# Optimization experiments

Hardware: AMD Instinct MI355X
Metric: run time of the kernel (lower is better)

Reference implementation:

```python
import jax, jax.numpy as jnp
import numpy as np

L = 4       # num_fourier_layers
W = 256     # width
NF = 256    # num_freq (no_low_freq)
B = 2       # batch size
N = 16384   # num_nodes per graph
E = 524288  # total edges (avg degree 16)
D_IN = 3    # darcy input features


def lin(x, w, b):
    # torch nn.Linear convention: w is (out, in)
    return x @ w.T + b


def layernorm(x, s, b):
    m = x.mean(-1, keepdims=True)
    v = x.var(-1, keepdims=True)
    return (x - m) / jnp.sqrt(v + 1e-5) * s + b


def setup_inputs() -> dict:
    key = jax.random.key(0)
    ks = jax.random.split(key, 16)
    s = lambda i, shape, sc=0.05: sc * jax.random.normal(ks[i], shape, jnp.float32)
    inp = {
        "x": jax.random.normal(ks[0], (B * N, D_IN), jnp.float32),
        "U": jax.random.normal(ks[1], (B, N, NF), jnp.float32) / np.float32(np.sqrt(N)),
        "edge_index": jax.random.randint(ks[2], (2, E), 0, B * N),
        "edge_weight": jax.random.uniform(ks[3], (E,), jnp.float32),
        "lif_embed": jax.random.normal(ks[4], (B * N, 16), jnp.float32),
        "p_w": s(5, (W, D_IN)), "p_b": jnp.zeros((W,), jnp.float32),
        # scale = 1/(in*out) * rand, per GraphFourierLayer
        "four_w": (1.0 / (W * W)) * jax.random.uniform(ks[6], (L, W, W, NF), jnp.float32),
        "w_w": s(7, (L, W, W)), "w_b": jnp.zeros((L, W), jnp.float32),
        "ln_s": jnp.ones((L, W), jnp.float32), "ln_b": jnp.zeros((L, W), jnp.float32),
        "lin_w": s(8, (L, W, W)), "lin_b": jnp.zeros((L, W), jnp.float32),
        "ew_w": s(9, (L, 16, 1)), "ew_b": jnp.zeros((L, 16), jnp.float32),
        "g1_w": s(10, (L, 3, 48)), "g1_b": jnp.zeros((L, 3), jnp.float32),
        "g2_w": s(11, (L, 1, 3)), "g2_b": jnp.zeros((L, 1), jnp.float32),
        "proj_w": s(12, (W, 2 * W)), "proj_b": jnp.zeros((W,), jnp.float32),
        "q1_w": s(13, (128, W)), "q1_b": jnp.zeros((128,), jnp.float32),
        "q2_w": s(14, (1, 128)), "q2_b": jnp.zeros((1,), jnp.float32),
    }
    return inp


def reference(x, U, edge_index, edge_weight, lif_embed,
              p_w, p_b, four_w, w_w, w_b, ln_s, ln_b,
              lin_w, lin_b, ew_w, ew_b, g1_w, g1_b, g2_w, g2_b,
              proj_w, proj_b, q1_w, q1_b, q2_w, q2_b):
    src = edge_index[0]  # edge_index_j (source)
    dst = edge_index[1]  # edge_index_i (target, aggr='add')
    h = lin(x, p_w, p_b)  # [B*N, W]

    for l in range(L):
        # --- GraphFourierLayer: batched spectral transform ---
        h3 = h.reshape(B, N, W)
        x_ft = jnp.einsum('bnf,bnw->bfw', U, h3)          # U^T x  -> [B, NF, W]
        out_ft = jnp.einsum('bfi,iof->bfo', x_ft, four_w[l])
        x1 = jnp.einsum('bnf,bfw->bnw', U, out_ft).reshape(B * N, W)
        xf = jax.nn.gelu(x1 + lin(h, w_w[l], w_b[l]), approximate=False)
        xf = layernorm(xf, ln_s[l], ln_b[l])

        # --- FrigateConv: gather -> edge MLP gate -> scatter-add -> L2 normalize ---
        xs = lin(h, lin_w[l], lin_b[l])
        ew = lin(edge_weight[:, None], ew_w[l], ew_b[l])  # [E, 16]
        gin = jnp.concatenate([ew, lif_embed[dst], lif_embed[src]], axis=1)  # [E, 48]
        g = jax.nn.sigmoid(lin(jax.nn.relu(lin(gin, g1_w[l], g1_b[l])), g2_w[l], g2_b[l]))
        msg = xs[src] * g                                  # [E, W]
        agg = jax.ops.segment_sum(msg, dst, num_segments=B * N)
        nrm = jnp.maximum(jnp.linalg.norm(agg, axis=-1, keepdims=True), 1e-12)
        xs = agg / nrm

        h = lin(jnp.concatenate([xf, xs], axis=1), proj_w, proj_b)

    out = lin(jax.nn.relu(lin(h, q1_w, q1_b)), q2_w, q2_b)  # q: MLP(W,1,128)
    return out
```

## Files before the change

kernel.cpp:

```cpp
#include <hip/hip_runtime.h>
#include <hip/hip_bf16.h>

#define B_ 2
#define N_ 16384
#define BN 32768
#define W_ 256
#define NF_ 256
#define E_ 524288
#define L_ 4
#define KS_ 32

typedef __attribute__((ext_vector_type(8))) short bf16x8;
typedef __attribute__((ext_vector_type(4))) float f32x4;

__device__ __forceinline__ unsigned short f2b(float x) {
    __hip_bfloat16 h = __float2bfloat16(x);
    return *reinterpret_cast<unsigned short*>(&h);
}
__device__ __forceinline__ float b2f(unsigned short u) {
    union { unsigned int i; float f; } c; c.i = ((unsigned int)u) << 16; return c.f;
}
__device__ __forceinline__ float geluf(float x) {
    return 0.5f * x * (1.0f + erff(x * 0.70710678118654752440f));
}

template<bool DUAL, int OUTM, bool BIAS, bool QHEAD = false, bool TROUT = false>
__global__ __launch_bounds__(256) void k_mfma_nt(
    const unsigned short* __restrict__ A1, int lda1, long A1o, long A1i,
    const unsigned short* __restrict__ B1, int ldb1, long B1o, long B1i, int K1,
    const unsigned short* __restrict__ A2, int lda2, long A2o,
    const unsigned short* __restrict__ B2, int ldb2, long B2o, int K2,
    void* __restrict__ Cv, int ldc, long Co, long Ci,
    unsigned short* __restrict__ CT,
    const float* __restrict__ bias,
    const float* __restrict__ qw, const float* __restrict__ q2b,
    float* __restrict__ qout, int zdiv)
{
    __shared__ unsigned short lds[16384];
    const int t = threadIdx.x;
    const int wid = t >> 6, lane = t & 63;
    const int wr = wid >> 1, wc = wid & 1;
    const int m0 = blockIdx.y * 128, n0 = blockIdx.x * 128;
    const int z = blockIdx.z;
    const int zo = z / zdiv, zi = z - zo * zdiv;
    A1 += zo * A1o + zi * A1i;
    B1 += zo * B1o + zi * B1i;
    if (DUAL) { A2 += zo * A2o; B2 += zo * B2o; }

    const int srow  = t >> 3;
    const int sgran = (t & 7) ^ (srow & 7);
    const int rlo   = lane & 15;
    const int hi    = lane >> 4;

    f32x4 acc[4][4] = {};

    const int nph = DUAL ? 2 : 1;
    for (int ph = 0; ph < nph; ++ph) {
        const unsigned short* A  = (DUAL && ph) ? A2 : A1;
        const unsigned short* Bp = (DUAL && ph) ? B2 : B1;
        const int lda = (DUAL && ph) ? lda2 : lda1;
        const int ldb = (DUAL && ph) ? ldb2 : ldb1;
        const int K   = (DUAL && ph) ? K2 : K1;
        for (int k0 = 0; k0 < K; k0 += 64) {
            __syncthreads();
            #pragma unroll
            for (int j = 0; j < 4; ++j) {
                const unsigned short* ga = A + (long)(m0 + j*32 + srow) * lda + k0 + sgran*8;
                __builtin_amdgcn_global_load_lds(
                    (const __attribute__((address_space(1))) void*)ga,
                    (__attribute__((address_space(3))) void*)&lds[(j*4 + wid) * 512],
                    16, 0, 0);
            }
            #pragma unroll
            for (int j = 0; j < 4; ++j) {
                const unsigned short* gb = Bp + (long)(n0 + j*32 + srow) * ldb + k0 + sgran*8;
                __builtin_amdgcn_global_load_lds(
                    (const __attribute__((address_space(1))) void*)gb,
                    (__attribute__((address_space(3))) void*)&lds[8192 + (j*4 + wid) * 512],
                    16, 0, 0);
            }
            __syncthreads();
            #pragma unroll
            for (int kk = 0; kk < 2; ++kk) {
                const int g8 = (((kk*4 + hi) ^ (lane & 7)) << 3);
                bf16x8 a[4], b[4];
                #pragma unroll
                for (int fm = 0; fm < 4; ++fm)
                    a[fm] = *(const bf16x8*)&lds[(wr*64 + fm*16 + rlo)*64 + g8];
                #pragma unroll
                for (int fn = 0; fn < 4; ++fn)
                    b[fn] = *(const bf16x8*)&lds[8192 + (wc*64 + fn*16 + rlo)*64 + g8];
                #pragma unroll
                for (int fm = 0; fm < 4; ++fm)
                    #pragma unroll
                    for (int fn = 0; fn < 4; ++fn)
                        acc[fm][fn] = __builtin_amdgcn_mfma_f32_16x16x32_bf16(
                            a[fm], b[fn], acc[fm][fn], 0, 0, 0);
            }
        }
    }

    const int mb = m0 + wr*64, nb = n0 + wc*64;
    if (QHEAD) {
        __syncthreads();
        float* rs = (float*)lds;
        if (t < 128) rs[t] = 0.f;
        __syncthreads();
        #pragma unroll
        for (int fm = 0; fm < 4; ++fm)
            #pragma unroll
            for (int r = 0; r < 4; ++r) {
                const int m_l = wr*64 + fm*16 + hi*4 + r;
                float part = 0.f;
                #pragma unroll
                for (int fn = 0; fn < 4; ++fn) {
                    const int n = nb + fn*16 + rlo;
                    part += fmaxf(acc[fm][fn][r] + bias[n], 0.f) * qw[n];
                }
                #pragma unroll
                for (int o = 8; o; o >>= 1) part += __shfl_xor(part, o);
                if (rlo == 0) atomicAdd(&rs[m_l], part);
            }
        __syncthreads();
        if (t < 128) qout[m0 + t] = rs[t] + q2b[0];
    } else if (OUTM == 1) {
        unsigned short* C = (unsigned short*)Cv + zo * Co + zi * Ci;
        #pragma unroll
        for (int fn = 0; fn < 4; ++fn) {
            const int n = nb + fn*16 + rlo;
            const float bv = BIAS ? bias[n] : 0.f;
            #pragma unroll
            for (int fm = 0; fm < 4; ++fm)
                #pragma unroll
                for (int r = 0; r < 4; ++r) {
                    const int m = mb + fm*16 + hi*4 + r;
                    C[(long)m*ldc + n] = f2b(acc[fm][fn][r] + bv);
                }
        }
        if (TROUT) {
            __syncthreads();
            unsigned short* wlds = &lds[wid * 4096];
            #pragma unroll
            for (int fm = 0; fm < 4; ++fm)
                #pragma unroll
                for (int r = 0; r < 4; ++r) {
                    const int m_l = fm*16 + hi*4 + r;
                    const int sw = (m_l & 7) << 3;
                    #pragma unroll
                    for (int fn = 0; fn < 4; ++fn) {
                        const int n_l = fn*16 + rlo;
                        const float bv = BIAS ? bias[nb + n_l] : 0.f;
                        wlds[m_l*64 + (n_l ^ sw)] = f2b(acc[fm][fn][r] + bv);
                    }
                }
            const int bb = mb >> 14, loc = mb & 16383;
            const int mq = lane & 15, nq = lane >> 4;
            #pragma unroll
            for (int p = 0; p < 16; ++p) {
                const int n_l = p*4 + nq;
                unsigned short v[4];
                #pragma unroll
                for (int j = 0; j < 4; ++j) {
                    const int m_l = mq*4 + j;
                    v[j] = wlds[m_l*64 + (n_l ^ ((m_l & 7) << 3))];
                }
                *(ushort4*)&CT[((long)bb*ldc + nb + n_l)*N_ + loc + mq*4] = *(ushort4*)v;
            }
        }
    } else {
        float* C = (float*)Cv + zo * Co + zi * Ci;
        #pragma unroll
        for (int fn = 0; fn < 4; ++fn) {
            const int n = nb + fn*16 + rlo;
            const float bv = BIAS ? bias[n] : 0.f;
            #pragma unroll
            for (int fm = 0; fm < 4; ++fm)
                #pragma unroll
                for (int r = 0; r < 4; ++r) {
                    const int m = mb + fm*16 + hi*4 + r;
                    C[(long)m*ldc + n] = acc[fm][fn][r] + bv;
                }
        }
    }
}

__global__ __launch_bounds__(256) void k_spec_xs(
    const unsigned short* __restrict__ hT, const unsigned short* __restrict__ UT,
    float* __restrict__ xft_part,
    const unsigned short* __restrict__ h, const unsigned short* __restrict__ linw,
    const float* __restrict__ lin_b, unsigned short* __restrict__ xs)
{
    __shared__ unsigned short lds[16384];
    const int t = threadIdx.x;
    const int wid = t >> 6, lane = t & 63;
    const int wr = wid >> 1, wc = wid & 1;
    const int srow  = t >> 3;
    const int sgran = (t & 7) ^ (srow & 7);
    const int rlo   = lane & 15;
    const int hi    = lane >> 4;
    const int blk = blockIdx.x;

    if (blk < 256) {
        const int bx = blk & 1, by = (blk >> 1) & 1, z = blk >> 2;
        const int zo = z / KS_, zi = z - zo * KS_;
        const unsigned short* A  = hT + (long)zo * W_ * N_ + (long)zi * (N_ / KS_);
        const unsigned short* Bp = UT + (long)zo * NF_ * N_ + (long)zi * (N_ / KS_);
        const int m0 = by * 128, n0 = bx * 128;
        f32x4 acc[4][4] = {};
        for (int k0 = 0; k0 < N_/KS_; k0 += 64) {
            __syncthreads();
            #pragma unroll
            for (int j = 0; j < 4; ++j) {
                const unsigned short* ga = A + (long)(m0 + j*32 + srow) * N_ + k0 + sgran*8;
                __builtin_amdgcn_global_load_lds(
                    (const __attribute__((address_space(1))) void*)ga,
                    (__attribute__((address_space(3))) void*)&lds[(j*4 + wid) * 512], 16, 0, 0);
                const unsigned short* gb = Bp + (long)(n0 + j*32 + srow) * N_ + k0 + sgran*8;
                __builtin_amdgcn_global_load_lds(
                    (const __attribute__((address_space(1))) void*)gb,
                    (__attribute__((address_space(3))) void*)&lds[8192 + (j*4 + wid) * 512], 16, 0, 0);
            }
            __syncthreads();
            #pragma unroll
            for (int kk = 0; kk < 2; ++kk) {
                const int g8 = (((kk*4 + hi) ^ (lane & 7)) << 3);
                bf16x8 a[4], b[4];
                #pragma unroll
                for (int fm = 0; fm < 4; ++fm)
                    a[fm] = *(const bf16x8*)&lds[(wr*64 + fm*16 + rlo)*64 + g8];
                #pragma unroll
                for (int fn = 0; fn < 4; ++fn)
                    b[fn] = *(const bf16x8*)&lds[8192 + (wc*64 + fn*16 + rlo)*64 + g8];
                #pragma unroll
                for (int fm = 0; fm < 4; ++fm)
                    #pragma unroll
                    for (int fn = 0; fn < 4; ++fn)
                        acc[fm][fn] = __builtin_amdgcn_mfma_f32_16x16x32_bf16(
                            a[fm], b[fn], acc[fm][fn], 0, 0, 0);
            }
        }
        float* C = xft_part + (long)zo * KS_ * 65536 + (long)zi * 65536;
        const int mb = m0 + wr*64, nb = n0 + wc*64;
        #pragma unroll
        for (int fn = 0; fn < 4; ++fn) {
            const int n = nb + fn*16 + rlo;
            #pragma unroll
            for (int fm = 0; fm < 4; ++fm)
                #pragma unroll
                for (int r = 0; r < 4; ++r) {
                    const int m = mb + fm*16 + hi*4 + r;
                    C[(long)m*NF_ + n] = acc[fm][fn][r];
                }
        }
    } else {
        const int idx = blk - 256;
        const int bx = idx & 1, by = idx >> 1;
        const int m0 = by * 128, n0 = bx * 128;
        f32x4 acc[4][4] = {};
        for (int k0 = 0; k0 < W_; k0 += 64) {
            __syncthreads();
            #pragma unroll
            for (int j = 0; j < 4; ++j) {
                const unsigned short* ga = h + (long)(m0 + j*32 + srow) * W_ + k0 + sgran*8;
                __builtin_amdgcn_global_load_lds(
                    (const __attribute__((address_space(1))) void*)ga,
                    (__attribute__((address_space(3))) void*)&lds[(j*4 + wid) * 512], 16, 0, 0);
                const unsigned short* gb = linw + (long)(n0 + j*32 + srow) * W_ + k0 + sgran*8;
                __builtin_amdgcn_global_load_lds(
                    (const __attribute__((address_space(1))) void*)gb,
                    (__attribute__((address_space(3))) void*)&lds[8192 + (j*4 + wid) * 512], 16, 0, 0);
            }
            __syncthreads();
            #pragma unroll
            for (int kk = 0; kk < 2; ++kk) {
                const int g8 = (((kk*4 + hi) ^ (lane & 7)) << 3);
                bf16x8 a[4], b[4];
                #pragma unroll
                for (int fm = 0; fm < 4; ++fm)
                    a[fm] = *(const bf16x8*)&lds[(wr*64 + fm*16 + rlo)*64 + g8];
                #pragma unroll
                for (int fn = 0; fn < 4; ++fn)
                    b[fn] = *(const bf16x8*)&lds[8192 + (wc*64 + fn*16 + rlo)*64 + g8];
                #pragma unroll
                for (int fm = 0; fm < 4; ++fm)
                    #pragma unroll
                    for (int fn = 0; fn < 4; ++fn)
                        acc[fm][fn] = __builtin_amdgcn_mfma_f32_16x16x32_bf16(
                            a[fm], b[fn], acc[fm][fn], 0, 0, 0);
            }
        }
        const int mb = m0 + wr*64, nb = n0 + wc*64;
        #pragma unroll
        for (int fn = 0; fn < 4; ++fn) {
            const int n = nb + fn*16 + rlo;
            const float lb = lin_b[n];
            #pragma unroll
            for (int fm = 0; fm < 4; ++fm)
                #pragma unroll
                for (int r = 0; r < 4; ++r) {
                    const int m = mb + fm*16 + hi*4 + r;
                    xs[(long)m*W_ + n] = f2b(acc[fm][fn][r] + lb);
                }
        }
    }
}

__global__ __launch_bounds__(256) void k_four_gate(
    const float* __restrict__ fw, const float* __restrict__ xftT,
    unsigned short* __restrict__ oftT,
    const int* __restrict__ offsets, const int* __restrict__ srcp,
    const float* __restrict__ ewt_p, const float* __restrict__ lif,
    const float* __restrict__ eww, const float* __restrict__ ewb,
    const float* __restrict__ g1w, const float* __restrict__ g1b,
    const float* __restrict__ g2w, const float* __restrict__ g2b,
    const unsigned short* __restrict__ xs, unsigned short* __restrict__ xsn)
{
    const int lane = threadIdx.x & 63;
    if (blockIdx.x < 256) {
        const int o = blockIdx.x, f = threadIdx.x;
        const float* fwp = fw + (long)o * NF_ + f;
        float a0 = 0.f, a1 = 0.f;
        #pragma unroll 8
        for (int i = 0; i < W_; ++i) {
            float w = fwp[(long)i * W_ * NF_];
            a0 = fmaf(xftT[i*NF_ + f], w, a0);
            a1 = fmaf(xftT[65536 + i*NF_ + f], w, a1);
        }
        oftT[o*NF_ + f] = f2b(a0);
        oftT[65536 + o*NF_ + f] = f2b(a1);
    } else {
        const int node = (blockIdx.x - 256) * 4 + (threadIdx.x >> 6);
        const int beg = offsets[node], end = offsets[node + 1];
        float lifd[16];
        #pragma unroll
        for (int j = 0; j < 16; ++j) lifd[j] = lif[node*16 + j];
        float a0=0.f, a1=0.f, a2=0.f, a3=0.f;
        for (int c0 = beg; c0 < end; c0 += 64) {
            const int p = c0 + lane;
            float gate = 0.f; int src = 0;
            if (p < end) {
                src = srcp[p];
                const float wv = ewt_p[p];
                float t0 = g1b[0], t1 = g1b[1], t2 = g1b[2];
                #pragma unroll
                for (int j = 0; j < 16; ++j) {
                    const float e0 = fmaf(wv, eww[j], ewb[j]);
                    const float l1 = lifd[j];
                    const float l2 = lif[src*16 + j];
                    t0 = fmaf(g1w[j], e0, t0);
                    t0 = fmaf(g1w[16 + j], l1, t0);
                    t0 = fmaf(g1w[32 + j], l2, t0);
                    t1 = fmaf(g1w[48 + j], e0, t1);
                    t1 = fmaf(g1w[64 + j], l1, t1);
                    t1 = fmaf(g1w[80 + j], l2, t1);
                    t2 = fmaf(g1w[96 + j], e0, t2);
                    t2 = fmaf(g1w[112 + j], l1, t2);
                    t2 = fmaf(g1w[128 + j], l2, t2);
                }
                float z = g2b[0];
                z = fmaf(g2w[0], fmaxf(t0, 0.f), z);
                z = fmaf(g2w[1], fmaxf(t1, 0.f), z);
                z = fmaf(g2w[2], fmaxf(t2, 0.f), z);
                gate = 1.f / (1.f + __expf(-z));
            }
            const int m = min(64, end - c0);
            for (int j = 0; j < m; ++j) {
                const float gv = __shfl(gate, j);
                const int   s  = __shfl(src, j);
                ushort4 v = *(const ushort4*)&xs[(long)s * W_ + lane * 4];
                a0 = fmaf(b2f(v.x), gv, a0);
                a1 = fmaf(b2f(v.y), gv, a1);
                a2 = fmaf(b2f(v.z), gv, a2);
                a3 = fmaf(b2f(v.w), gv, a3);
            }
        }
        float s = a0*a0 + a1*a1 + a2*a2 + a3*a3;
        #pragma unroll
        for (int o = 32; o; o >>= 1) s += __shfl_xor(s, o);
        float inv = 1.f / fmaxf(sqrtf(s), 1e-12f);
        ushort4 r = {f2b(a0*inv), f2b(a1*inv), f2b(a2*inv), f2b(a3*inv)};
        *(ushort4*)(xsn + (long)node * W_ + lane * 4) = r;
    }
}

__global__ __launch_bounds__(256) void k_prologue(
    const float* __restrict__ w_w, const float* __restrict__ lin_w,
    const float* __restrict__ proj_w, const float* __restrict__ q1_w,
    unsigned short* __restrict__ wwb, unsigned short* __restrict__ linwb,
    unsigned short* __restrict__ projwb, unsigned short* __restrict__ q1wb,
    const float* __restrict__ U, unsigned short* __restrict__ UT, unsigned short* __restrict__ UL,
    const float* __restrict__ x, const float* __restrict__ pw, const float* __restrict__ pb,
    unsigned short* __restrict__ h, unsigned short* __restrict__ hT)
{
    __shared__ unsigned short tile[64][72];
    const int blk = blockIdx.x;
    const int t = threadIdx.x;
    if (blk < 672) {
        const float* s; unsigned short* d; long base;
        if (blk < 256)      { s = w_w;    d = wwb;    base = (long)blk * 1024; }
        else if (blk < 512) { s = lin_w;  d = linwb;  base = (long)(blk-256) * 1024; }
        else if (blk < 640) { s = proj_w; d = projwb; base = (long)(blk-512) * 1024; }
        else                { s = q1_w;   d = q1wb;   base = (long)(blk-640) * 1024; }
        long i = base + (long)t * 4;
        float4 v = *(const float4*)&s[i];
        ushort4 u = {f2b(v.x), f2b(v.y), f2b(v.z), f2b(v.w)};
        *(ushort4*)&d[i] = u;
    } else if (blk < 2720) {
        const int lb = blk - 672;
        const int b = lb >> 10;
        const int rem = lb & 1023;
        const int cy = rem >> 2, cx = rem & 3;
        const float* src = U + (long)b * N_ * NF_;
        unsigned short* dT = UT + (long)b * N_ * NF_;
        unsigned short* dL = UL + (long)b * N_ * NF_;
        const int r0 = cy * 64, c0 = cx * 64;
        const int lr = t >> 4, lc4 = (t & 15) * 4;
        #pragma unroll
        for (int p = 0; p < 4; ++p) {
            int r = p*16 + lr;
            float4 v = *(const float4*)&src[(long)(r0+r)*NF_ + c0 + lc4];
            ushort4 u = {f2b(v.x), f2b(v.y), f2b(v.z), f2b(v.w)};
            *(ushort4*)&dL[(long)(r0+r)*NF_ + c0 + lc4] = u;
            tile[r][lc4+0]=u.x; tile[r][lc4+1]=u.y; tile[r][lc4+2]=u.z; tile[r][lc4+3]=u.w;
        }
        __syncthreads();
        #pragma unroll
        for (int p = 0; p < 4; ++p) {
            int c = p*16 + lr;
            ushort4 u = {tile[lc4+0][c], tile[lc4+1][c], tile[lc4+2][c], tile[lc4+3][c]};
            *(ushort4*)&dT[(long)(c0+c)*N_ + r0 + lc4] = u;
        }
    } else {
        const int lb = blk - 2720;
        const int b = lb >> 10;
        const int rem = lb & 1023;
        const int ry = rem >> 2, rx = rem & 3;
        const int r0 = ry * 64, c0 = rx * 64;
        const int lr = t >> 4, lc4 = (t & 15) * 4;
        float pwv[12], pbv4[4];
        #pragma unroll
        for (int j = 0; j < 4; ++j) {
            const int w = c0 + lc4 + j;
            pwv[j*3+0] = pw[w*3+0]; pwv[j*3+1] = pw[w*3+1]; pwv[j*3+2] = pw[w*3+2];
            pbv4[j] = pb[w];
        }
        #pragma unroll
        for (int p = 0; p < 4; ++p) {
            const int r = p*16 + lr;
            const float* xr = x + (long)(b*N_ + r0 + r) * 3;
            const float x0 = xr[0], x1 = xr[1], x2 = xr[2];
            ushort4 u;
            u.x = f2b(fmaf(x0,pwv[0],fmaf(x1,pwv[1],fmaf(x2,pwv[2],pbv4[0]))));
            u.y = f2b(fmaf(x0,pwv[3],fmaf(x1,pwv[4],fmaf(x2,pwv[5],pbv4[1]))));
            u.z = f2b(fmaf(x0,pwv[6],fmaf(x1,pwv[7],fmaf(x2,pwv[8],pbv4[2]))));
            u.w = f2b(fmaf(x0,pwv[9],fmaf(x1,pwv[10],fmaf(x2,pwv[11],pbv4[3]))));
            *(ushort4*)&h[(long)(b*N_ + r0 + r)*W_ + c0 + lc4] = u;
            tile[r][lc4+0]=u.x; tile[r][lc4+1]=u.y; tile[r][lc4+2]=u.z; tile[r][lc4+3]=u.w;
        }
        __syncthreads();
        #pragma unroll
        for (int p = 0; p < 4; ++p) {
            const int c = p*16 + lr;
            ushort4 u = {tile[lc4+0][c], tile[lc4+1][c], tile[lc4+2][c], tile[lc4+3][c]};
            *(ushort4*)&hT[((long)b*W_ + c0 + c)*N_ + r0 + lc4] = u;
        }
    }
}

__global__ __launch_bounds__(256) void k_reduce_ks(
    const float* __restrict__ part, float* __restrict__ outp)
{
    int idx = blockIdx.x * 256 + threadIdx.x;
    int b = idx >> 16, rem = idx & 65535;
    const float* p = part + (long)b * KS_ * 65536 + rem;
    float s = 0.f;
    #pragma unroll 16
    for (int k = 0; k < KS_; ++k) s += p[(long)k * 65536];
    outp[idx] = s;
}

__global__ __launch_bounds__(256) void k_gelu_ln(
    const unsigned short* __restrict__ xf, unsigned short* __restrict__ out,
    const float* __restrict__ wb, const float* __restrict__ lns, const float* __restrict__ lnb)
{
    const int node = blockIdx.x * 4 + (threadIdx.x >> 6);
    const int lane = threadIdx.x & 63;
    ushort4 v4 = *(const ushort4*)(xf + (long)node*W_ + lane*4);
    float4 bb = *(const float4*)(wb + lane*4);
    float e0 = geluf(b2f(v4.x)+bb.x), e1 = geluf(b2f(v4.y)+bb.y);
    float e2 = geluf(b2f(v4.z)+bb.z), e3 = geluf(b2f(v4.w)+bb.w);
    float s  = e0+e1+e2+e3;
    float s2 = e0*e0+e1*e1+e2*e2+e3*e3;
    #pragma unroll
    for (int o = 32; o; o >>= 1) { s += __shfl_xor(s, o); s2 += __shfl_xor(s2, o); }
    float mean = s * (1.0f/W_);
    float var  = s2 * (1.0f/W_) - mean*mean;
    float inv = rsqrtf(var + 1e-5f);
    float4 sc = *(const float4*)(lns + lane*4);
    float4 bi = *(const float4*)(lnb + lane*4);
    ushort4 o4;
    o4.x = f2b((e0-mean)*inv*sc.x + bi.x);
    o4.y = f2b((e1-mean)*inv*sc.y + bi.y);
    o4.z = f2b((e2-mean)*inv*sc.z + bi.z);
    o4.w = f2b((e3-mean)*inv*sc.w + bi.w);
    *(ushort4*)(out + (long)node*W_ + lane*4) = o4;
}

__global__ __launch_bounds__(256) void k_hist(const int* __restrict__ ei, int* __restrict__ count) {
    int e = blockIdx.x * 256 + threadIdx.x;
    atomicAdd(&count[ei[E_ + e]], 1);
}
__global__ __launch_bounds__(1024) void k_scan(const int* __restrict__ count, int* __restrict__ offsets) {
    __shared__ int sums[1024];
    const int t = threadIdx.x;
    const int base = t * 32;
    int s = 0;
    #pragma unroll
    for (int i = 0; i < 32; ++i) s += count[base + i];
    sums[t] = s;
    __syncthreads();
    for (int off = 1; off < 1024; off <<= 1) {
        int v = (t >= off) ? sums[t - off] : 0;
        __syncthreads();
        sums[t] += v;
        __syncthreads();
    }
    int run = (t == 0) ? 0 : sums[t - 1];
    #pragma unroll
    for (int i = 0; i < 32; ++i) { offsets[base + i] = run; run += count[base + i]; }
    if (t == 1023) offsets[BN] = run;
}
__global__ __launch_bounds__(256) void k_place(
    const int* __restrict__ ei, const float* __restrict__ ewt,
    const int* __restrict__ offsets, int* __restrict__ cursor,
    int* __restrict__ srcp, float* __restrict__ ewt_p)
{
    int e = blockIdx.x * 256 + threadIdx.x;
    int dst = ei[E_ + e];
    int pos = offsets[dst] + atomicAdd(&cursor[dst], 1);
    srcp[pos] = ei[e];
    ewt_p[pos] = ewt[e];
}

extern "C" void kernel_launch(void* const* d_in, const int* in_sizes, int n_in,
                              void* d_out, int out_size, void* d_ws, size_t ws_size,
                              hipStream_t stream)
{
    const float* x      = (const float*)d_in[0];
    const float* U      = (const float*)d_in[1];
    const int*   ei     = (const int*)  d_in[2];
    const float* ewt    = (const float*)d_in[3];
    const float* lif    = (const float*)d_in[4];
    const float* p_w    = (const float*)d_in[5];
    const float* p_b    = (const float*)d_in[6];
    const float* four_w = (const float*)d_in[7];
    const float* w_w    = (const float*)d_in[8];
    const float* w_b    = (const float*)d_in[9];
    const float* ln_s   = (const float*)d_in[10];
    const float* ln_b   = (const float*)d_in[11];
    const float* lin_w  = (const float*)d_in[12];
    const float* lin_b  = (const float*)d_in[13];
    const float* ew_w   = (const float*)d_in[14];
    const float* ew_b   = (const float*)d_in[15];
    const float* g1_w   = (const float*)d_in[16];
    const float* g1_b   = (const float*)d_in[17];
    const float* g2_w   = (const float*)d_in[18];
    const float* g2_b   = (const float*)d_in[19];
    const float* proj_w = (const float*)d_in[20];
    const float* proj_b = (const float*)d_in[21];
    const float* q1_w   = (const float*)d_in[22];
    const float* q1_b   = (const float*)d_in[23];
    const float* q2_w   = (const float*)d_in[24];
    const float* q2_b   = (const float*)d_in[25];

    char* wsb = (char*)d_ws;
    size_t off = 0;
    auto alloc = [&](size_t bytes) -> void* {
        void* p = wsb + off; off += (bytes + 255) & ~(size_t)255; return p;
    };
    float* xft_part  = (float*)alloc((size_t)B_ * KS_ * 65536 * 4);
    float* xftT      = (float*)alloc((size_t)B_ * 65536 * 4);
    unsigned short* h_bf   = (unsigned short*)alloc((size_t)BN * W_ * 2);
    unsigned short* hT_bf  = (unsigned short*)alloc((size_t)BN * W_ * 2);
    unsigned short* U_bf   = (unsigned short*)alloc((size_t)BN * NF_ * 2);
    unsigned short* UT_bf  = (unsigned short*)alloc((size_t)BN * NF_ * 2);
    unsigned short* xfg    = (unsigned short*)alloc((size_t)BN * W_ * 2);
    unsigned short* xf_bf  = (unsigned short*)alloc((size_t)BN * W_ * 2);
    unsigned short* xs_bf  = (unsigned short*)alloc((size_t)BN * W_ * 2);
    unsigned short* xsn_bf = (unsigned short*)alloc((size_t)BN * W_ * 2);
    unsigned short* oftT_bf= (unsigned short*)alloc((size_t)B_ * 65536 * 2);
    unsigned short* wwb    = (unsigned short*)alloc((size_t)L_ * W_ * W_ * 2);
    unsigned short* linwb  = (unsigned short*)alloc((size_t)L_ * W_ * W_ * 2);
    unsigned short* projwb = (unsigned short*)alloc((size_t)W_ * 2 * W_ * 2);
    unsigned short* q1wb   = (unsigned short*)alloc((size_t)128 * W_ * 2);
    int*   srcp    = (int*)alloc((size_t)E_ * 4);
    float* ewt_p   = (float*)alloc((size_t)E_ * 4);
    int*   count   = (int*)alloc((size_t)BN * 4);
    int*   cursor  = (int*)alloc((size_t)BN * 4);
    int*   offsets = (int*)alloc((size_t)(BN + 1) * 4);

    hipMemsetAsync(count, 0, (size_t)2 * BN * 4, stream);
    k_hist<<<E_/256, 256, 0, stream>>>(ei, count);
    k_scan<<<1, 1024, 0, stream>>>(count, offsets);
    k_place<<<E_/256, 256, 0, stream>>>(ei, ewt, offsets, cursor, srcp, ewt_p);

    k_prologue<<<4768, 256, 0, stream>>>(
        w_w, lin_w, proj_w, q1_w, wwb, linwb, projwb, q1wb,
        U, UT_bf, U_bf,
        x, p_w, p_b, h_bf, hT_bf);

    for (int l = 0; l < L_; ++l) {
        k_spec_xs<<<768, 256, 0, stream>>>(
            hT_bf, UT_bf, xft_part,
            h_bf, linwb + (long)l*W_*W_, lin_b + l*W_, xs_bf);
        k_reduce_ks<<<(B_*65536)/256, 256, 0, stream>>>(xft_part, xftT);
        k_four_gate<<<256 + BN/4, 256, 0, stream>>>(
            four_w + (long)l*W_*W_*NF_, xftT, oftT_bf,
            offsets, srcp, ewt_p, lif,
            ew_w + l*16, ew_b + l*16, g1_w + l*144, g1_b + l*3,
            g2_w + l*3, g2_b + l, xs_bf, xsn_bf);
        k_mfma_nt<true,1,false><<<dim3(2, N_/128, B_), 256, 0, stream>>>(
            U_bf, NF_, (long)N_*NF_, 0,
            oftT_bf, NF_, (long)65536, 0, NF_,
            h_bf, W_, (long)N_*W_,
            wwb + (long)l*W_*W_, W_, 0, W_,
            xfg, W_, (long)N_*W_, 0,
            nullptr, nullptr, nullptr, nullptr, nullptr, 1);
        k_gelu_ln<<<BN/4, 256, 0, stream>>>(xfg, xf_bf, w_b + l*W_, ln_s + l*W_, ln_b + l*W_);
        if (l < 3) {
            k_mfma_nt<true,1,true,false,true><<<dim3(2, BN/128, 1), 256, 0, stream>>>(
                xf_bf, W_, 0, 0,
                projwb, 2*W_, 0, 0, W_,
                xsn_bf, W_, 0,
                projwb + W_, 2*W_, 0, W_,
                h_bf, W_, 0, 0,
                hT_bf, proj_b, nullptr, nullptr, nullptr, 1);
        } else {
            k_mfma_nt<true,1,true><<<dim3(2, BN/128, 1), 256, 0, stream>>>(
                xf_bf, W_, 0, 0,
                projwb, 2*W_, 0, 0, W_,
                xsn_bf, W_, 0,
                projwb + W_, 2*W_, 0, W_,
                h_bf, W_, 0, 0,
                nullptr, proj_b, nullptr, nullptr, nullptr, 1);
        }
    }
    k_mfma_nt<false,0,true,true><<<dim3(1, BN/128, 1), 256, 0, stream>>>(
        h_bf, W_, 0, 0,
        q1wb, W_, 0, 0, W_,
        nullptr, 0, 0, nullptr, 0, 0, 0,
        nullptr, 128, 0, 0,
        nullptr, q1_b, q2_w, q2_b, (float*)d_out, 1);
}
```

Measured before the change: 698.1 us.

## Split gather-gate work across fourier-mix and xf GEMM kernels for overlap

```diff
diff --git a/kernel.cpp b/kernel.cpp
--- a/kernel.cpp
+++ b/kernel.cpp
@@ -22,6 +22,67 @@
 }
 __device__ __forceinline__ float geluf(float x) {
     return 0.5f * x * (1.0f + erff(x * 0.70710678118654752440f));
+}
+
+__device__ __forceinline__ void gate_agg_node(
+    int node, int lane,
+    const int* __restrict__ offsets, const int* __restrict__ srcp,
+    const float* __restrict__ ewt_p, const float* __restrict__ lif,
+    const float* __restrict__ eww, const float* __restrict__ ewb,
+    const float* __restrict__ g1w, const float* __restrict__ g1b,
+    const float* __restrict__ g2w, const float* __restrict__ g2b,
+    const unsigned short* __restrict__ xs, unsigned short* __restrict__ xsn)
+{
+    const int beg = offsets[node], end = offsets[node + 1];
+    float lifd[16];
+    #pragma unroll
+    for (int j = 0; j < 16; ++j) lifd[j] = lif[node*16 + j];
+    float a0=0.f, a1=0.f, a2=0.f, a3=0.f;
+    for (int c0 = beg; c0 < end; c0 += 64) {
+        const int p = c0 + lane;
+        float gate = 0.f; int src = 0;
+        if (p < end) {
+            src = srcp[p];
+            const float wv = ewt_p[p];
+            float t0 = g1b[0], t1 = g1b[1], t2 = g1b[2];
+            #pragma unroll
+            for (int j = 0; j < 16; ++j) {
+                const float e0 = fmaf(wv, eww[j], ewb[j]);
+                const float l1 = lifd[j];
+                const float l2 = lif[src*16 + j];
+                t0 = fmaf(g1w[j], e0, t0);
+                t0 = fmaf(g1w[16 + j], l1, t0);
+                t0 = fmaf(g1w[32 + j], l2, t0);
+                t1 = fmaf(g1w[48 + j], e0, t1);
+                t1 = fmaf(g1w[64 + j], l1, t1);
+                t1 = fmaf(g1w[80 + j], l2, t1);
+                t2 = fmaf(g1w[96 + j], e0, t2);
+                t2 = fmaf(g1w[112 + j], l1, t2);
+                t2 = fmaf(g1w[128 + j], l2, t2);
+            }
+            float z = g2b[0];
+            z = fmaf(g2w[0], fmaxf(t0, 0.f), z);
+            z = fmaf(g2w[1], fmaxf(t1, 0.f), z);
+            z = fmaf(g2w[2], fmaxf(t2, 0.f), z);
+            gate = 1.f / (1.f + __expf(-z));
+        }
+        const int m = min(64, end - c0);
+        for (int j = 0; j < m; ++j) {
+            const float gv = __shfl(gate, j);
+            const int   s  = __shfl(src, j);
+            ushort4 v = *(const ushort4*)&xs[(long)s * W_ + lane * 4];
+            a0 = fmaf(b2f(v.x), gv, a0);
+            a1 = fmaf(b2f(v.y), gv, a1);
+            a2 = fmaf(b2f(v.z), gv, a2);
+            a3 = fmaf(b2f(v.w), gv, a3);
+        }
+    }
+    float s = a0*a0 + a1*a1 + a2*a2 + a3*a3;
+    #pragma unroll
+    for (int o = 32; o; o >>= 1) s += __shfl_xor(s, o);
+    float inv = 1.f / fmaxf(sqrtf(s), 1e-12f);
+    ushort4 r = {f2b(a0*inv), f2b(a1*inv), f2b(a2*inv), f2b(a3*inv)};
+    *(ushort4*)(xsn + (long)node * W_ + lane * 4) = r;
 }
 
 template<bool DUAL, int OUTM, bool BIAS, bool QHEAD = false, bool TROUT = false>
@@ -330,56 +391,93 @@
         oftT[65536 + o*NF_ + f] = f2b(a1);
     } else {
         const int node = (blockIdx.x - 256) * 4 + (threadIdx.x >> 6);
-        const int beg = offsets[node], end = offsets[node + 1];
-        float lifd[16];
-        #pragma unroll
-        for (int j = 0; j < 16; ++j) lifd[j] = lif[node*16 + j];
-        float a0=0.f, a1=0.f, a2=0.f, a3=0.f;
-        for (int c0 = beg; c0 < end; c0 += 64) {
-            const int p = c0 + lane;
-            float gate = 0.f; int src = 0;
-            if (p < end) {
-                src = srcp[p];
-                const float wv = ewt_p[p];
-                float t0 = g1b[0], t1 = g1b[1], t2 = g1b[2];
-                #pragma unroll
-                for (int j = 0; j < 16; ++j) {
-                    const float e0 = fmaf(wv, eww[j], ewb[j]);
-                    const float l1 = lifd[j];
-                    const float l2 = lif[src*16 + j];
-                    t0 = fmaf(g1w[j], e0, t0);
-                    t0 = fmaf(g1w[16 + j], l1, t0);
-                    t0 = fmaf(g1w[32 + j], l2, t0);
-                    t1 = fmaf(g1w[48 + j], e0, t1);
-                    t1 = fmaf(g1w[64 + j], l1, t1);
-                    t1 = fmaf(g1w[80 + j], l2, t1);
-                    t2 = fmaf(g1w[96 + j], e0, t2);
-                    t2 = fmaf(g1w[112 + j], l1, t2);
-                    t2 = fmaf(g1w[128 + j], l2, t2);
-                }
-                float z = g2b[0];
-                z = fmaf(g2w[0], fmaxf(t0, 0.f), z);
-                z = fmaf(g2w[1], fmaxf(t1, 0.f), z);
-                z = fmaf(g2w[2], fmaxf(t2, 0.f), z);
-                gate = 1.f / (1.f + __expf(-z));
-            }
-            const int m = min(64, end - c0);
-            for (int j = 0; j < m; ++j) {
-                const float gv = __shfl(gate, j);
-                const int   s  = __shfl(src, j);
-                ushort4 v = *(const ushort4*)&xs[(long)s * W_ + lane * 4];
-                a0 = fmaf(b2f(v.x), gv, a0);
-                a1 = fmaf(b2f(v.y), gv, a1);
-                a2 = fmaf(b2f(v.z), gv, a2);
-                a3 = fmaf(b2f(v.w), gv, a3);
-            }
-        }
-        float s = a0*a0 + a1*a1 + a2*a2 + a3*a3;
-        #pragma unroll
-        for (int o = 32; o; o >>= 1) s += __shfl_xor(s, o);
-        float inv = 1.f / fmaxf(sqrtf(s), 1e-12f);
-        ushort4 r = {f2b(a0*inv), f2b(a1*inv), f2b(a2*inv), f2b(a3*inv)};
-        *(ushort4*)(xsn + (long)node * W_ + lane * 4) = r;
+        gate_agg_node(node, lane, offsets, srcp, ewt_p, lif,
+                      eww, ewb, g1w, g1b, g2w, g2b, xs, xsn);
+    }
+}
+
+__global__ __launch_bounds__(256) void k_xf_gate(
+    const unsigned short* __restrict__ Ubf, const unsigned short* __restrict__ oftT,
+    const unsigned short* __restrict__ h, const unsigned short* __restrict__ ww,
+    unsigned short* __restrict__ xfg,
+    const int* __restrict__ offsets, const int* __restrict__ srcp,
+    const float* __restrict__ ewt_p, const float* __restrict__ lif,
+    const float* __restrict__ eww, const float* __restrict__ ewb,
+    const float* __restrict__ g1w, const float* __restrict__ g1b,
+    const float* __restrict__ g2w, const float* __restrict__ g2b,
+    const unsigned short* __restrict__ xs, unsigned short* __restrict__ xsn)
+{
+    __shared__ unsigned short lds[16384];
+    const int blk = blockIdx.x;
+    const int t = threadIdx.x;
+    const int lane = t & 63;
+    if (blk < 512) {
+        const int wid = t >> 6;
+        const int wr = wid >> 1, wc = wid & 1;
+        const int bx = blk & 1, by = (blk >> 1) & 127, b = blk >> 8;
+        const int m0 = by * 128, n0 = bx * 128;
+        const unsigned short* A1 = Ubf  + (long)b * N_ * NF_;
+        const unsigned short* B1 = oftT + (long)b * 65536;
+        const unsigned short* A2 = h    + (long)b * N_ * W_;
+        const int srow  = t >> 3;
+        const int sgran = (t & 7) ^ (srow & 7);
+        const int rlo   = lane & 15;
+        const int hi    = lane >> 4;
+        f32x4 acc[4][4] = {};
+        #pragma unroll
+        for (int ph = 0; ph < 2; ++ph) {
+            const unsigned short* A  = ph ? A2 : A1;
+            const unsigned short* Bp = ph ? ww : B1;
+            for (int k0 = 0; k0 < 256; k0 += 64) {
+                __syncthreads();
+                #pragma unroll
+                for (int j = 0; j < 4; ++j) {
+                    const unsigned short* ga = A + (long)(m0 + j*32 + srow) * 256 + k0 + sgran*8;
+                    __builtin_amdgcn_global_load_lds(
+                        (const __attribute__((address_space(1))) void*)ga,
+                        (__attribute__((address_space(3))) void*)&lds[(j*4 + wid) * 512], 16, 0, 0);
+                    const unsigned short* gb = Bp + (long)(n0 + j*32 + srow) * 256 + k0 + sgran*8;
+                    __builtin_amdgcn_global_load_lds(
+                        (const __attribute__((address_space(1))) void*)gb,
+                        (__attribute__((address_space(3))) void*)&lds[8192 + (j*4 + wid) * 512], 16, 0, 0);
+                }
+                __syncthreads();
+                #pragma unroll
+                for (int kk = 0; kk < 2; ++kk) {
+                    const int g8 = (((kk*4 + hi) ^ (lane & 7)) << 3);
+                    bf16x8 a[4], b[4];
+                    #pragma unroll
+                    for (int fm = 0; fm < 4; ++fm)
+                        a[fm] = *(const bf16x8*)&lds[(wr*64 + fm*16 + rlo)*64 + g8];
+                    #pragma unroll
+                    for (int fn = 0; fn < 4; ++fn)
+                        b[fn] = *(const bf16x8*)&lds[8192 + (wc*64 + fn*16 + rlo)*64 + g8];
+                    #pragma unroll
+                    for (int fm = 0; fm < 4; ++fm)
+                        #pragma unroll
+                        for (int fn = 0; fn < 4; ++fn)
+                            acc[fm][fn] = __builtin_amdgcn_mfma_f32_16x16x32_bf16(
+                                a[fm], b[fn], acc[fm][fn], 0, 0, 0);
+                }
+            }
+        }
+        unsigned short* C = xfg + (long)b * N_ * W_;
+        const int mb = m0 + wr*64, nb = n0 + wc*64;
+        #pragma unroll
+        for (int fn = 0; fn < 4; ++fn) {
+            const int n = nb + fn*16 + rlo;
+            #pragma unroll
+            for (int fm = 0; fm < 4; ++fm)
+                #pragma unroll
+                for (int r = 0; r < 4; ++r) {
+                    const int m = mb + fm*16 + hi*4 + r;
+                    C[(long)m*W_ + n] = f2b(acc[fm][fn][r]);
+                }
+        }
+    } else {
+        const int node = BN/2 + (blk - 512) * 4 + (t >> 6);
+        gate_agg_node(node, lane, offsets, srcp, ewt_p, lif,
+                      eww, ewb, g1w, g1b, g2w, g2b, xs, xsn);
     }
 }
 
@@ -614,18 +712,16 @@
             hT_bf, UT_bf, xft_part,
             h_bf, linwb + (long)l*W_*W_, lin_b + l*W_, xs_bf);
         k_reduce_ks<<<(B_*65536)/256, 256, 0, stream>>>(xft_part, xftT);
-        k_four_gate<<<256 + BN/4, 256, 0, stream>>>(
+        k_four_gate<<<256 + BN/8, 256, 0, stream>>>(
             four_w + (long)l*W_*W_*NF_, xftT, oftT_bf,
             offsets, srcp, ewt_p, lif,
             ew_w + l*16, ew_b + l*16, g1_w + l*144, g1_b + l*3,
             g2_w + l*3, g2_b + l, xs_bf, xsn_bf);
-        k_mfma_nt<true,1,false><<<dim3(2, N_/128, B_), 256, 0, stream>>>(
-            U_bf, NF_, (long)N_*NF_, 0,
-            oftT_bf, NF_, (long)65536, 0, NF_,
-            h_bf, W_, (long)N_*W_,
-            wwb + (long)l*W_*W_, W_, 0, W_,
-            xfg, W_, (long)N_*W_, 0,
-            nullptr, nullptr, nullptr, nullptr, nullptr, 1);
+        k_xf_gate<<<512 + BN/8, 256, 0, stream>>>(
+            U_bf, oftT_bf, h_bf, wwb + (long)l*W_*W_, xfg,
+            offsets, srcp, ewt_p, lif,
+            ew_w + l*16, ew_b + l*16, g1_w + l*144, g1_b + l*3,
+            g2_w + l*3, g2_b + l, xs_bf, xsn_bf);
         k_gelu_ln<<<BN/4, 256, 0, stream>>>(xfg, xf_bf, w_b + l*W_, ln_s + l*W_, ln_b + l*W_);
         if (l < 3) {
             k_mfma_nt<true,1,true,false,true><<<dim3(2, BN/128, 1), 256, 0, stream>>>(
```

Result: slower. 872.0 us (+24.9%).

## Fuse spectral-inverse GEMM with GELU and LayerNorm into one full-row kernel

Applied to the files above, without the earlier changes.

```diff
diff --git a/kernel.cpp b/kernel.cpp
--- a/kernel.cpp
+++ b/kernel.cpp
@@ -182,6 +182,116 @@
                 }
         }
     }
+}
+
+__global__ __launch_bounds__(256) void k_xf_ln(
+    const unsigned short* __restrict__ Ubf, const unsigned short* __restrict__ oftT,
+    const unsigned short* __restrict__ h, const unsigned short* __restrict__ ww,
+    const float* __restrict__ wb, const float* __restrict__ lns, const float* __restrict__ lnb,
+    unsigned short* __restrict__ xf)
+{
+    __shared__ unsigned short lds[24576];
+    const int t = threadIdx.x;
+    const int wid = t >> 6, lane = t & 63;
+    const int m0 = blockIdx.x * 128;
+    const int b = blockIdx.y;
+    Ubf  += (long)b * N_ * NF_;
+    oftT += (long)b * 65536;
+    h    += (long)b * N_ * W_;
+
+    const int srow  = t >> 3;
+    const int sgran = (t & 7) ^ (srow & 7);
+    const int rlo   = lane & 15;
+    const int hi    = lane >> 4;
+
+    f32x4 acc[8][4] = {};
+
+    #pragma unroll
+    for (int ph = 0; ph < 2; ++ph) {
+        const unsigned short* A  = ph ? h  : Ubf;
+        const unsigned short* Bp = ph ? ww : oftT;
+        for (int k0 = 0; k0 < 256; k0 += 64) {
+            __syncthreads();
+            #pragma unroll
+            for (int j = 0; j < 4; ++j) {
+                const unsigned short* ga = A + (long)(m0 + j*32 + srow) * 256 + k0 + sgran*8;
+                __builtin_amdgcn_global_load_lds(
+                    (const __attribute__((address_space(1))) void*)ga,
+                    (__attribute__((address_space(3))) void*)&lds[(j*4 + wid) * 512], 16, 0, 0);
+            }
+            #pragma unroll
+            for (int j = 0; j < 8; ++j) {
+                const unsigned short* gb = Bp + (long)(j*32 + srow) * 256 + k0 + sgran*8;
+                __builtin_amdgcn_global_load_lds(
+                    (const __attribute__((address_space(1))) void*)gb,
+                    (__attribute__((address_space(3))) void*)&lds[8192 + (j*4 + wid) * 512], 16, 0, 0);
+            }
+            __syncthreads();
+            #pragma unroll
+            for (int kk = 0; kk < 2; ++kk) {
+                const int g8 = (((kk*4 + hi) ^ (lane & 7)) << 3);
+                bf16x8 bfr[4];
+                #pragma unroll
+                for (int fn = 0; fn < 4; ++fn)
+                    bfr[fn] = *(const bf16x8*)&lds[8192 + (wid*64 + fn*16 + rlo)*64 + g8];
+                #pragma unroll
+                for (int fm = 0; fm < 8; ++fm) {
+                    bf16x8 a = *(const bf16x8*)&lds[(fm*16 + rlo)*64 + g8];
+                    #pragma unroll
+                    for (int fn = 0; fn < 4; ++fn)
+                        acc[fm][fn] = __builtin_amdgcn_mfma_f32_16x16x32_bf16(
+                            a, bfr[fn], acc[fm][fn], 0, 0, 0);
+                }
+            }
+        }
+    }
+
+    float wbv[4], lsv[4], lbv[4];
+    #pragma unroll
+    for (int fn = 0; fn < 4; ++fn) {
+        const int c = wid*64 + fn*16 + rlo;
+        wbv[fn] = wb[c]; lsv[fn] = lns[c]; lbv[fn] = lnb[c];
+    }
+    __syncthreads();
+    float* sums  = (float*)lds;
+    float* sumsq = (float*)lds + 512;
+    #pragma unroll
+    for (int fm = 0; fm < 8; ++fm)
+        #pragma unroll
+        for (int r = 0; r < 4; ++r) {
+            float s = 0.f, s2 = 0.f;
+            #pragma unroll
+            for (int fn = 0; fn < 4; ++fn) {
+                const float g = geluf(acc[fm][fn][r] + wbv[fn]);
+                acc[fm][fn][r] = g;
+                s += g; s2 += g*g;
+            }
+            #pragma unroll
+            for (int o = 1; o < 16; o <<= 1) { s += __shfl_xor(s, o); s2 += __shfl_xor(s2, o); }
+            if (rlo == 0) {
+                const int row = fm*16 + hi*4 + r;
+                sums [row*4 + wid] = s;
+                sumsq[row*4 + wid] = s2;
+            }
+        }
+    __syncthreads();
+    #pragma unroll
+    for (int fm = 0; fm < 8; ++fm)
+        #pragma unroll
+        for (int r = 0; r < 4; ++r) {
+            const int row = fm*16 + hi*4 + r;
+            const float s  = sums [row*4+0] + sums [row*4+1] + sums [row*4+2] + sums [row*4+3];
+            const float s2 = sumsq[row*4+0] + sumsq[row*4+1] + sumsq[row*4+2] + sumsq[row*4+3];
+            const float mean = s * (1.0f/W_);
+            const float var  = s2 * (1.0f/W_) - mean*mean;
+            const float inv  = rsqrtf(var + 1e-5f);
+            const long mrow = (long)(b*N_ + m0 + row) * W_;
+            #pragma unroll
+            for (int fn = 0; fn < 4; ++fn) {
+                const int c = wid*64 + fn*16 + rlo;
+                xf[mrow + c] = f2b((acc[fm][fn][r] - mean)*inv*lsv[fn] + lbv[fn]);
+            }
+        }
 }
 
 __global__ __launch_bounds__(256) void k_spec_xs(
@@ -479,33 +589,6 @@
     outp[idx] = s;
 }
 
-__global__ __launch_bounds__(256) void k_gelu_ln(
-    const unsigned short* __restrict__ xf, unsigned short* __restrict__ out,
-    const float* __restrict__ wb, const float* __restrict__ lns, const float* __restrict__ lnb)
-{
-    const int node = blockIdx.x * 4 + (threadIdx.x >> 6);
-    const int lane = threadIdx.x & 63;
-    ushort4 v4 = *(const ushort4*)(xf + (long)node*W_ + lane*4);
-    float4 bb = *(const float4*)(wb + lane*4);
-    float e0 = geluf(b2f(v4.x)+bb.x), e1 = geluf(b2f(v4.y)+bb.y);
-    float e2 = geluf(b2f(v4.z)+bb.z), e3 = geluf(b2f(v4.w)+bb.w);
-    float s  = e0+e1+e2+e3;
-    float s2 = e0*e0+e1*e1+e2*e2+e3*e3;
-    #pragma unroll
-    for (int o = 32; o; o >>= 1) { s += __shfl_xor(s, o); s2 += __shfl_xor(s2, o); }
-    float mean = s * (1.0f/W_);
-    float var  = s2 * (1.0f/W_) - mean*mean;
-    float inv = rsqrtf(var + 1e-5f);
-    float4 sc = *(const float4*)(lns + lane*4);
-    float4 bi = *(const float4*)(lnb + lane*4);
-    ushort4 o4;
-    o4.x = f2b((e0-mean)*inv*sc.x + bi.x);
-    o4.y = f2b((e1-mean)*inv*sc.y + bi.y);
-    o4.z = f2b((e2-mean)*inv*sc.z + bi.z);
-    o4.w = f2b((e3-mean)*inv*sc.w + bi.w);
-    *(ushort4*)(out + (long)node*W_ + lane*4) = o4;
-}
-
 __global__ __launch_bounds__(256) void k_hist(const int* __restrict__ ei, int* __restrict__ count) {
     int e = blockIdx.x * 256 + threadIdx.x;
     atomicAdd(&count[ei[E_ + e]], 1);
@@ -584,7 +667,6 @@
     unsigned short* hT_bf  = (unsigned short*)alloc((size_t)BN * W_ * 2);
     unsigned short* U_bf   = (unsigned short*)alloc((size_t)BN * NF_ * 2);
     unsigned short* UT_bf  = (unsigned short*)alloc((size_t)BN * NF_ * 2);
-    unsigned short* xfg    = (unsigned short*)alloc((size_t)BN * W_ * 2);
     unsigned short* xf_bf  = (unsigned short*)alloc((size_t)BN * W_ * 2);
     unsigned short* xs_bf  = (unsigned short*)alloc((size_t)BN * W_ * 2);
     unsigned short* xsn_bf = (unsigned short*)alloc((size_t)BN * W_ * 2);
@@ -619,14 +701,9 @@
             offsets, srcp, ewt_p, lif,
             ew_w + l*16, ew_b + l*16, g1_w + l*144, g1_b + l*3,
             g2_w + l*3, g2_b + l, xs_bf, xsn_bf);
-        k_mfma_nt<true,1,false><<<dim3(2, N_/128, B_), 256, 0, stream>>>(
-            U_bf, NF_, (long)N_*NF_, 0,
-            oftT_bf, NF_, (long)65536, 0, NF_,
-            h_bf, W_, (long)N_*W_,
-            wwb + (long)l*W_*W_, W_, 0, W_,
-            xfg, W_, (long)N_*W_, 0,
-            nullptr, nullptr, nullptr, nullptr, nullptr, 1);
-        k_gelu_ln<<<BN/4, 256, 0, stream>>>(xfg, xf_bf, w_b + l*W_, ln_s + l*W_, ln_b + l*W_);
+        k_xf_ln<<<dim3(N_/128, B_), 256, 0, stream>>>(
+            U_bf, oftT_bf, h_bf, wwb + (long)l*W_*W_,
+            w_b + l*W_, ln_s + l*W_, ln_b + l*W_, xf_bf);
         if (l < 3) {
             k_mfma_nt<true,1,true,false,true><<<dim3(2, BN/128, 1), 256, 0, stream>>>(
                 xf_bf, W_, 0, 0,
```

Result: slower. 1.029 ms (+47.4%).
